# Kernel optimization log

Measured on AMD Instinct MI355X. Metric: run time of the kernel, lower is better.

Reference implementation:

```python
import jax, jax.numpy as jnp
import numpy as np
import math

NUM_LABELS = 8
D_MODEL = 1024
NUM_HEADS = 16
D_PADDED = math.ceil(D_MODEL / NUM_HEADS) * NUM_HEADS  # 1024
D_HEAD = D_PADDED // NUM_HEADS  # 64
B, N = 4, 2048


def setup_inputs() -> dict:
    key = jax.random.key(0)
    ks = jax.random.split(key, 7)
    X = jax.random.normal(ks[0], (B, N, D_MODEL), dtype=jnp.float32)
    L = jax.random.randint(ks[1], (B, N), 0, NUM_LABELS, dtype=jnp.int32)
    # per-label QKV linear params (stored as x @ W + b layout)
    s_in = 1.0 / math.sqrt(D_MODEL)
    Wqkv = jax.random.uniform(ks[2], (NUM_LABELS, D_MODEL, 3 * D_PADDED), jnp.float32, -s_in, s_in)
    bqkv = jax.random.uniform(ks[3], (NUM_LABELS, 3 * D_PADDED), jnp.float32, -s_in, s_in)
    s_p = 1.0 / math.sqrt(D_PADDED)
    Wproj = jax.random.uniform(ks[4], (D_PADDED, D_MODEL), jnp.float32, -s_p, s_p)
    bproj = jax.random.uniform(ks[5], (D_MODEL,), jnp.float32, -s_p, s_p)
    return {"X": X, "L": L, "Wqkv": Wqkv, "bqkv": bqkv, "Wproj": Wproj, "bproj": bproj}


def reference(X, L, Wqkv, bqkv, Wproj, bproj):
    Bb, Nn, _ = X.shape
    # Per-label dense QKV projection, routed by label mask (matches original
    # per-label loop; X_masked zeroing is a no-op on selected positions).
    qkv = jnp.zeros((Bb, Nn, 3 * D_PADDED), dtype=X.dtype)
    for l in range(NUM_LABELS):
        m = (L == l)[..., None]  # [B, N, 1]
        qkv_l = jnp.einsum('bnd,do->bno', X, Wqkv[l]) + bqkv[l]
        qkv = jnp.where(m, qkv_l, qkv)
    q, k, v = jnp.split(qkv, 3, axis=-1)
    # [B, H, N, Dh]
    q = q.reshape(Bb, Nn, NUM_HEADS, D_HEAD).transpose(0, 2, 1, 3)
    k = k.reshape(Bb, Nn, NUM_HEADS, D_HEAD).transpose(0, 2, 1, 3)
    v = v.reshape(Bb, Nn, NUM_HEADS, D_HEAD).transpose(0, 2, 1, 3)
    scores = jnp.einsum('bhnd,bhmd->bhnm', q, k) / math.sqrt(D_HEAD)
    probs = jax.nn.softmax(scores, axis=-1)
    out = jnp.einsum('bhnm,bhmd->bhnd', probs, v)
    out = out.transpose(0, 2, 1, 3).reshape(Bb, Nn, D_PADDED)
    return jnp.einsum('bnd,do->bno', out, Wproj) + bproj
```

## Files before the change

kernel.cpp:

```cpp
#include <hip/hip_runtime.h>
#include <math.h>

#define BATCH 4
#define SEQ   2048
#define TOK   (BATCH * SEQ)
#define DM    1024
#define DP    1024
#define NH    16
#define DH    64
#define NLAB  8
#define QKV_C 3072
#define PADL  1152
#define PROWS (NLAB * PADL)
#define GP    72

typedef __attribute__((ext_vector_type(8))) short bf16x8;
typedef __attribute__((ext_vector_type(4))) float f32x4;

typedef const __attribute__((address_space(1))) void* gas_ptr;
typedef __attribute__((address_space(3))) void* las_ptr;

__device__ __forceinline__ short f2bf(float f) {
  union { float f; unsigned u; } v; v.f = f;
  unsigned r = v.u + 0x7FFF + ((v.u >> 16) & 1);
  return (short)(r >> 16);
}

__device__ __forceinline__ unsigned cvt_pk_bf16(float lo, float hi) {
  unsigned r;
  asm("v_cvt_pk_bf16_f32 %0, %1, %2" : "=v"(r) : "v"(lo), "v"(hi));
  return r;
}

__device__ __forceinline__ float fast_exp2(float x) {
#if __has_builtin(__builtin_amdgcn_exp2f)
  return __builtin_amdgcn_exp2f(x);
#else
  return exp2f(x);
#endif
}

__global__ void build_lists_k(const int* __restrict__ L, int* __restrict__ sorted,
                              int* __restrict__ rowmap) {
  __shared__ int cnt[NLAB], off[NLAB], cur[NLAB];
  int tid = threadIdx.x;
  if (tid < NLAB) cnt[tid] = 0;
  __syncthreads();
  for (int i = tid; i < TOK; i += 256) atomicAdd(&cnt[L[i]], 1);
  __syncthreads();
  if (tid == 0) {
    int o = 0;
    for (int l = 0; l < NLAB; ++l) { off[l] = o; cur[l] = o; o += cnt[l]; }
  }
  __syncthreads();
  for (int i = tid; i < TOK; i += 256) {
    int l = L[i];
    sorted[atomicAdd(&cur[l], 1)] = i;
  }
  __threadfence();
  __syncthreads();
  for (int p = tid; p < PROWS; p += 256) {
    int l = p / PADL, i = p - l * PADL;
    rowmap[p] = (i < cnt[l]) ? sorted[off[l] + i] : -1;
  }
}

__global__ __launch_bounds__(256) void xg_k(const float* __restrict__ X,
                                            const int* __restrict__ rowmap,
                                            short* __restrict__ Xg) {
  int p = blockIdx.x;
  int t = rowmap[p];
  int c = threadIdx.x << 2;
  short* dst = Xg + (size_t)p * DM + c;
  if (t >= 0) {
    float4 v = *(const float4*)(X + (size_t)t * DM + c);
    short tmp[4] = { f2bf(v.x), f2bf(v.y), f2bf(v.z), f2bf(v.w) };
    *(uint2*)dst = *(uint2*)tmp;
  } else {
    uint2 z; z.x = 0u; z.y = 0u;
    *(uint2*)dst = z;
  }
}

__global__ __launch_bounds__(256) void wt_k(const float* __restrict__ src,
                                            short* __restrict__ dst,
                                            int K, int N) {
  __shared__ float Ts[64][65];
  int m = blockIdx.z;
  src += (size_t)m * K * N;
  dst += (size_t)m * (size_t)N * K;
  int n0 = blockIdx.x * 64, k0 = blockIdx.y * 64;
  int tid = threadIdx.x;
  int r = tid >> 4;
  int c = (tid & 15) << 2;
  #pragma unroll
  for (int it = 0; it < 4; ++it) {
    float4 v = *(const float4*)(src + (size_t)(k0 + r + it * 16) * N + n0 + c);
    Ts[c + 0][r + it * 16] = v.x;
    Ts[c + 1][r + it * 16] = v.y;
    Ts[c + 2][r + it * 16] = v.z;
    Ts[c + 3][r + it * 16] = v.w;
  }
  __syncthreads();
  int n = tid >> 2, ks = (tid & 3) << 4;
  short tmp[16];
  #pragma unroll
  for (int j = 0; j < 16; ++j) tmp[j] = f2bf(Ts[n][ks + j]);
  *(bf16x8*)(dst + (size_t)(n0 + n) * K + k0 + ks)     = *(bf16x8*)&tmp[0];
  *(bf16x8*)(dst + (size_t)(n0 + n) * K + k0 + ks + 8) = *(bf16x8*)&tmp[8];
}

__global__ __launch_bounds__(256) void qkv_mfma_k(
    const short* __restrict__ Xg, const short* __restrict__ Wt,
    const float* __restrict__ bqkv, const int* __restrict__ rowmap,
    short* __restrict__ qkvb) {
  __shared__ short As[128 * 64];
  __shared__ short Bs[128 * 64];
  int bx = blockIdx.x, by = blockIdx.y;
  int lab = by / 9;
  int pr0 = by * 128;
  int n0  = bx * 128;
  const short* W = Wt + (size_t)lab * QKV_C * DM;

  int tid  = threadIdx.x;
  int lane = tid & 63, w = tid >> 6;
  int wm = w >> 1, wn = w & 1;
  int col = lane & 15, quad = lane >> 4;

  int lrow = lane >> 3;
  int lcol = (lane & 7) << 3;

  const short* aSrc = Xg + (size_t)(pr0 + w * 32 + lrow) * DM + lcol;
  const short* bSrc = W  + (size_t)(n0  + w * 32 + lrow) * DM + lcol;

  f32x4 acc[4][4];
  #pragma unroll
  for (int mi = 0; mi < 4; ++mi)
    #pragma unroll
    for (int ni = 0; ni < 4; ++ni) acc[mi][ni] = (f32x4){0.f, 0.f, 0.f, 0.f};

  for (int k0 = 0; k0 < DM; k0 += 64) {
    __syncthreads();
    #pragma unroll
    for (int it = 0; it < 4; ++it) {
      __builtin_amdgcn_global_load_lds(
          (gas_ptr)(aSrc + (size_t)(it * 8) * DM + k0),
          (las_ptr)&As[(w * 32 + it * 8) * 64], 16, 0, 0);
      __builtin_amdgcn_global_load_lds(
          (gas_ptr)(bSrc + (size_t)(it * 8) * DM + k0),
          (las_ptr)&Bs[(w * 32 + it * 8) * 64], 16, 0, 0);
    }
    __syncthreads();
    #pragma unroll
    for (int ks = 0; ks < 2; ++ks) {
      bf16x8 a[4], b[4];
      #pragma unroll
      for (int mi = 0; mi < 4; ++mi)
        a[mi] = *(bf16x8*)&As[(wm * 64 + mi * 16 + col) * 64 + ks * 32 + (quad << 3)];
      #pragma unroll
      for (int ni = 0; ni < 4; ++ni)
        b[ni] = *(bf16x8*)&Bs[(wn * 64 + ni * 16 + col) * 64 + ks * 32 + (quad << 3)];
      #pragma unroll
      for (int mi = 0; mi < 4; ++mi)
        #pragma unroll
        for (int ni = 0; ni < 4; ++ni)
          acc[mi][ni] = __builtin_amdgcn_mfma_f32_16x16x32_bf16(a[mi], b[ni], acc[mi][ni], 0, 0, 0);
    }
  }

  float scale = (bx < 8) ? (0.125f * 1.44269504f) : 1.0f;
  const float* bias = bqkv + lab * QKV_C;
  #pragma unroll
  for (int mi = 0; mi < 4; ++mi) {
    #pragma unroll
    for (int r = 0; r < 4; ++r) {
      int prow = pr0 + wm * 64 + mi * 16 + (quad << 2) + r;
      int t2 = rowmap[prow];
      if (t2 < 0) continue;
      #pragma unroll
      for (int ni = 0; ni < 4; ++ni) {
        int gn = n0 + wn * 64 + ni * 16 + col;
        float v = (acc[mi][ni][r] + bias[gn]) * scale;
        qkvb[(size_t)t2 * QKV_C + gn] = f2bf(v);
      }
    }
  }
}

__global__ __launch_bounds__(256) void vtb_k(const short* __restrict__ qkvb,
                                             short* __restrict__ VTg) {
  __shared__ short T[64 * GP];
  int n0 = blockIdx.x * 64, h = blockIdx.y, b = blockIdx.z;
  int tid = threadIdx.x;
  int r = tid >> 2, cb = tid & 3;
  {
    const short* src = qkvb + ((size_t)(b * SEQ + n0 + r)) * QKV_C + 2 * DP + h * DH + (cb << 4);
    int scc = ((cb + (r >> 4)) & 3) << 4;
    *(bf16x8*)&T[r * GP + scc]     = *(const bf16x8*)(src);
    *(bf16x8*)&T[r * GP + scc + 8] = *(const bf16x8*)(src + 8);
  }
  __syncthreads();
  int d = tid >> 2, nc = (tid & 3) << 4;
  int sc2 = (((d >> 4) + (nc >> 4)) & 3) << 4;
  short tmp[16];
  #pragma unroll
  for (int j = 0; j < 16; ++j) tmp[j] = T[(nc + j) * GP + sc2 + (d & 15)];
  short* dst = VTg + ((size_t)(b * NH + h) * DH + d) * SEQ + n0 + nc;
  *(bf16x8*)&dst[0] = *(bf16x8*)&tmp[0];
  *(bf16x8*)&dst[8] = *(bf16x8*)&tmp[8];
}

__global__ __launch_bounds__(256) void attn_k(short* __restrict__ qkvb,
                                              const short* __restrict__ VTg) {
  int qt = blockIdx.x, h = blockIdx.y, b = blockIdx.z;
  __shared__ short Ks[64 * GP];
  __shared__ short VT[64 * GP];
  __shared__ short Ps[128 * GP];

  int tid  = threadIdx.x;
  int lane = tid & 63;
  int w    = tid >> 6;
  int col  = lane & 15;
  int quad = lane >> 4;

  size_t rowbase = (size_t)b * SEQ;
  int hoff = h * DH;
  int sr = tid >> 2;
  int sc = (tid & 3) << 4;

  const short* ksrc = qkvb + (rowbase + sr) * QKV_C + DP + hoff + sc;
  const short* vsrc = VTg + ((size_t)(b * NH + h) * DH + sr) * SEQ + sc;

  bf16x8 qf0[2], qf1[2];
  {
    const short* q0 = qkvb + (rowbase + qt * 128 + (w << 4) + col) * QKV_C + hoff + (quad << 3);
    const short* q1 = q0 + (size_t)64 * QKV_C;
    qf0[0] = *(const bf16x8*)(q0);
    qf0[1] = *(const bf16x8*)(q0 + 32);
    qf1[0] = *(const bf16x8*)(q1);
    qf1[1] = *(const bf16x8*)(q1 + 32);
  }

  {
    bf16x8 ka = *(const bf16x8*)(ksrc);
    bf16x8 kb = *(const bf16x8*)(ksrc + 8);
    bf16x8 va = *(const bf16x8*)(vsrc);
    bf16x8 vb = *(const bf16x8*)(vsrc + 8);
    *(bf16x8*)&Ks[sr * GP + sc]     = ka;
    *(bf16x8*)&Ks[sr * GP + sc + 8] = kb;
    *(bf16x8*)&VT[sr * GP + sc]     = va;
    *(bf16x8*)&VT[sr * GP + sc + 8] = vb;
  }
  __syncthreads();

  float m_0 = -1e30f, l_0 = 0.f, m_1 = -1e30f, l_1 = 0.f;
  f32x4 o0[4], o1[4];
  #pragma unroll
  for (int nd = 0; nd < 4; ++nd) {
    o0[nd] = (f32x4){0.f, 0.f, 0.f, 0.f};
    o1[nd] = (f32x4){0.f, 0.f, 0.f, 0.f};
  }

  short* ps0 = &Ps[((w << 4) + col) * GP];
  short* ps1 = &Ps[(64 + (w << 4) + col) * GP];

  auto softmax_strip = [&](f32x4* s, float& m_, float& l_, f32x4* o, short* psrow) {
    f32x4 t0, t1;
    #pragma unroll
    for (int i = 0; i < 4; ++i) { t0[i] = fmaxf(s[0][i], s[1][i]); t1[i] = fmaxf(s[2][i], s[3][i]); }
    #pragma unroll
    for (int i = 0; i < 4; ++i) t0[i] = fmaxf(t0[i], t1[i]);
    float mx = fmaxf(fmaxf(t0[0], t0[1]), fmaxf(t0[2], t0[3]));
    if (!__all(mx - m_ <= 8.f)) {
      float mxr = fmaxf(mx, __shfl_xor(mx, 16));
      mxr = fmaxf(mxr, __shfl_xor(mxr, 32));
      float mnew  = fmaxf(m_, mxr);
      float alpha = fast_exp2(m_ - mnew);
      l_ *= alpha;
      #pragma unroll
      for (int nd = 0; nd < 4; ++nd)
        #pragma unroll
        for (int r = 0; r < 4; ++r) o[nd][r] *= alpha;
      m_ = mnew;
    }
    float p[4][4];
    #pragma unroll
    for (int nj = 0; nj < 4; ++nj)
      #pragma unroll
      for (int r = 0; r < 4; ++r) p[nj][r] = fast_exp2(s[nj][r] - m_);
    float rs = 0.f;
    #pragma unroll
    for (int nj = 0; nj < 4; ++nj)
      rs += (p[nj][0] + p[nj][1]) + (p[nj][2] + p[nj][3]);
    l_ += rs;
    #pragma unroll
    for (int nj = 0; nj < 4; ++nj) {
      uint2 u;
      u.x = cvt_pk_bf16(p[nj][0], p[nj][1]);
      u.y = cvt_pk_bf16(p[nj][2], p[nj][3]);
      *(uint2*)&psrow[nj * 16 + (quad << 2)] = u;
    }
  };

  auto compute_tile = [&]() {
    f32x4 s0[4], s1[4];
    #pragma unroll
    for (int nj = 0; nj < 4; ++nj) {
      s0[nj] = (f32x4){0.f, 0.f, 0.f, 0.f};
      s1[nj] = (f32x4){0.f, 0.f, 0.f, 0.f};
    }
    __builtin_amdgcn_s_setprio(1);
    #pragma unroll
    for (int ks = 0; ks < 2; ++ks) {
      #pragma unroll
      for (int nj = 0; nj < 4; ++nj) {
        bf16x8 aK = *(bf16x8*)&Ks[((nj << 4) + col) * GP + (ks << 5) + (quad << 3)];
        s0[nj] = __builtin_amdgcn_mfma_f32_16x16x32_bf16(aK, qf0[ks], s0[nj], 0, 0, 0);
        s1[nj] = __builtin_amdgcn_mfma_f32_16x16x32_bf16(aK, qf1[ks], s1[nj], 0, 0, 0);
      }
    }
    __builtin_amdgcn_s_setprio(0);
    softmax_strip(s0, m_0, l_0, o0, ps0);
    softmax_strip(s1, m_1, l_1, o1, ps1);
    __builtin_amdgcn_s_setprio(1);
    #pragma unroll
    for (int ks = 0; ks < 2; ++ks) {
      bf16x8 bP0 = *(bf16x8*)&ps0[(ks << 5) + (quad << 3)];
      bf16x8 bP1 = *(bf16x8*)&ps1[(ks << 5) + (quad << 3)];
      #pragma unroll
      for (int nd = 0; nd < 4; ++nd) {
        bf16x8 aV = *(bf16x8*)&VT[((nd << 4) + col) * GP + (ks << 5) + (quad << 3)];
        o0[nd] = __builtin_amdgcn_mfma_f32_16x16x32_bf16(aV, bP0, o0[nd], 0, 0, 0);
        o1[nd] = __builtin_amdgcn_mfma_f32_16x16x32_bf16(aV, bP1, o1[nd], 0, 0, 0);
      }
    }
    __builtin_amdgcn_s_setprio(0);
  };

  for (int kt = 0; kt < SEQ / 64 - 1; ++kt) {
    const short* kn = ksrc + (size_t)(kt + 1) * 64 * QKV_C;
    const short* vn = vsrc + (size_t)(kt + 1) * 64;
    bf16x8 ka = *(const bf16x8*)(kn);
    bf16x8 kb = *(const bf16x8*)(kn + 8);
    bf16x8 va = *(const bf16x8*)(vn);
    bf16x8 vb = *(const bf16x8*)(vn + 8);

    compute_tile();
    __syncthreads();
    *(bf16x8*)&Ks[sr * GP + sc]     = ka;
    *(bf16x8*)&Ks[sr * GP + sc + 8] = kb;
    *(bf16x8*)&VT[sr * GP + sc]     = va;
    *(bf16x8*)&VT[sr * GP + sc + 8] = vb;
    __syncthreads();
  }
  compute_tile();

  float lt0 = l_0 + __shfl_xor(l_0, 16);
  lt0 += __shfl_xor(lt0, 32);
  float lt1 = l_1 + __shfl_xor(l_1, 16);
  lt1 += __shfl_xor(lt1, 32);
  #pragma unroll
  for (int s = 0; s < 2; ++s) {
    float inv = 1.f / (s ? lt1 : lt0);
    f32x4* o = s ? o1 : o0;
    size_t row = rowbase + qt * 128 + s * 64 + (w << 4) + col;
    #pragma unroll
    for (int nd = 0; nd < 4; ++nd) {
      uint2 u;
      u.x = cvt_pk_bf16(o[nd][0] * inv, o[nd][1] * inv);
      u.y = cvt_pk_bf16(o[nd][2] * inv, o[nd][3] * inv);
      *(uint2*)(qkvb + row * QKV_C + hoff + (nd << 4) + (quad << 2)) = u;
    }
  }
}

__global__ __launch_bounds__(256) void proj_mfma_k(
    const short* __restrict__ Ab, const short* __restrict__ Wt,
    const float* __restrict__ bias, float* __restrict__ out) {
  __shared__ short As[128 * 64];
  __shared__ short Bs[128 * 64];
  int n0 = blockIdx.x * 128, m0 = blockIdx.y * 128;

  int tid  = threadIdx.x;
  int lane = tid & 63, w = tid >> 6;
  int wm = w >> 1, wn = w & 1;
  int col = lane & 15, quad = lane >> 4;

  int lrow = lane >> 3;
  int lcol = (lane & 7) << 3;

  const short* aSrc = Ab + (size_t)(m0 + w * 32 + lrow) * QKV_C + lcol;
  const short* bSrc = Wt + (size_t)(n0 + w * 32 + lrow) * DP + lcol;

  f32x4 acc[4][4];
  #pragma unroll
  for (int mi = 0; mi < 4; ++mi)
    #pragma unroll
    for (int ni = 0; ni < 4; ++ni) acc[mi][ni] = (f32x4){0.f, 0.f, 0.f, 0.f};

  for (int k0 = 0; k0 < DP; k0 += 64) {
    __syncthreads();
    #pragma unroll
    for (int it = 0; it < 4; ++it) {
      __builtin_amdgcn_global_load_lds(
          (gas_ptr)(aSrc + (size_t)(it * 8) * QKV_C + k0),
          (las_ptr)&As[(w * 32 + it * 8) * 64], 16, 0, 0);
      __builtin_amdgcn_global_load_lds(
          (gas_ptr)(bSrc + (size_t)(it * 8) * DP + k0),
          (las_ptr)&Bs[(w * 32 + it * 8) * 64], 16, 0, 0);
    }
    __syncthreads();
    #pragma unroll
    for (int ks = 0; ks < 2; ++ks) {
      bf16x8 a[4], b[4];
      #pragma unroll
      for (int mi = 0; mi < 4; ++mi)
        a[mi] = *(bf16x8*)&As[(wm * 64 + mi * 16 + col) * 64 + ks * 32 + (quad << 3)];
      #pragma unroll
      for (int ni = 0; ni < 4; ++ni)
        b[ni] = *(bf16x8*)&Bs[(wn * 64 + ni * 16 + col) * 64 + ks * 32 + (quad << 3)];
      #pragma unroll
      for (int mi = 0; mi < 4; ++mi)
        #pragma unroll
        for (int ni = 0; ni < 4; ++ni)
          acc[mi][ni] = __builtin_amdgcn_mfma_f32_16x16x32_bf16(a[mi], b[ni], acc[mi][ni], 0, 0, 0);
    }
  }

  #pragma unroll
  for (int mi = 0; mi < 4; ++mi) {
    #pragma unroll
    for (int r = 0; r < 4; ++r) {
      int m = m0 + wm * 64 + mi * 16 + (quad << 2) + r;
      #pragma unroll
      for (int ni = 0; ni < 4; ++ni) {
        int gn = n0 + wn * 64 + ni * 16 + col;
        out[(size_t)m * DM + gn] = acc[mi][ni][r] + bias[gn];
      }
    }
  }
}

extern "C" void kernel_launch(void* const* d_in, const int* in_sizes, int n_in,
                              void* d_out, int out_size, void* d_ws, size_t ws_size,
                              hipStream_t stream) {
  (void)in_sizes; (void)n_in; (void)out_size; (void)ws_size;
  const float* X     = (const float*)d_in[0];
  const int*   L     = (const int*)d_in[1];
  const float* Wqkv  = (const float*)d_in[2];
  const float* bqkv  = (const float*)d_in[3];
  const float* Wproj = (const float*)d_in[4];
  const float* bproj = (const float*)d_in[5];
  float* out = (float*)d_out;

  char* ws = (char*)d_ws;
  short* qkvb    = (short*)ws;
  short* Wqkv_t  = (short*)(ws + (size_t)TOK * QKV_C * 2);
  short* Wproj_t = (short*)(ws + (size_t)TOK * QKV_C * 2
                               + (size_t)NLAB * QKV_C * DM * 2);
  int* sorted = (int*)((char*)Wproj_t + (size_t)DP * DM * 2);
  int* rowmap = sorted + TOK;
  short* Xg = (short*)(rowmap + PROWS);
  short* VTg = Wqkv_t;

  build_lists_k<<<dim3(1), dim3(256), 0, stream>>>(L, sorted, rowmap);
  xg_k<<<dim3(PROWS), dim3(256), 0, stream>>>(X, rowmap, Xg);
  wt_k<<<dim3(QKV_C / 64, DM / 64, NLAB), dim3(256), 0, stream>>>(Wqkv, Wqkv_t, DM, QKV_C);
  wt_k<<<dim3(DM / 64, DP / 64, 1), dim3(256), 0, stream>>>(Wproj, Wproj_t, DP, DM);
  qkv_mfma_k<<<dim3(QKV_C / 128, PROWS / 128), dim3(256), 0, stream>>>(
      Xg, Wqkv_t, bqkv, rowmap, qkvb);
  vtb_k<<<dim3(SEQ / 64, NH, BATCH), dim3(256), 0, stream>>>(qkvb, VTg);
  attn_k<<<dim3(SEQ / 128, NH, BATCH), dim3(256), 0, stream>>>(qkvb, VTg);
  proj_mfma_k<<<dim3(DM / 128, TOK / 128), dim3(256), 0, stream>>>(
      qkvb, Wproj_t, bproj, out);
}
```

Before: 481.6 us.

## Double-buffer LDS tiles and swizzle block order in QKV and projection GEMMs

Both MFMA GEMM kernels now keep two LDS buffers per operand. They prefetch the next K-tile with global_load_lds while computing on the current one, and sync only once per iteration. This hides global-load latency behind MFMA work. The block index is also remapped so that consecutive blocks are spread across the grid, which is meant to improve L2 reuse or XCD distribution. LDS use doubles to 64KB per block, which may reduce occupancy.

```diff
diff --git a/kernel.cpp b/kernel.cpp
--- a/kernel.cpp
+++ b/kernel.cpp
@@ -114,9 +114,11 @@
     const short* __restrict__ Xg, const short* __restrict__ Wt,
     const float* __restrict__ bqkv, const int* __restrict__ rowmap,
     short* __restrict__ qkvb) {
-  __shared__ short As[128 * 64];
-  __shared__ short Bs[128 * 64];
-  int bx = blockIdx.x, by = blockIdx.y;
+  __shared__ short As[2][128 * 64];
+  __shared__ short Bs[2][128 * 64];
+  int flat = blockIdx.y * 24 + blockIdx.x;
+  int swz  = (flat & 7) * 216 + (flat >> 3);
+  int bx = swz % 24, by = swz / 24;
   int lab = by / 9;
   int pr0 = by * 128;
   int n0  = bx * 128;
@@ -139,33 +141,48 @@
     #pragma unroll
     for (int ni = 0; ni < 4; ++ni) acc[mi][ni] = (f32x4){0.f, 0.f, 0.f, 0.f};
 
+  #pragma unroll
+  for (int it = 0; it < 4; ++it) {
+    __builtin_amdgcn_global_load_lds(
+        (gas_ptr)(aSrc + (size_t)(it * 8) * DM),
+        (las_ptr)&As[0][(w * 32 + it * 8) * 64], 16, 0, 0);
+    __builtin_amdgcn_global_load_lds(
+        (gas_ptr)(bSrc + (size_t)(it * 8) * DM),
+        (las_ptr)&Bs[0][(w * 32 + it * 8) * 64], 16, 0, 0);
+  }
+  __syncthreads();
+
+  int cur = 0;
   for (int k0 = 0; k0 < DM; k0 += 64) {
-    __syncthreads();
-    #pragma unroll
-    for (int it = 0; it < 4; ++it) {
-      __builtin_amdgcn_global_load_lds(
-          (gas_ptr)(aSrc + (size_t)(it * 8) * DM + k0),
-          (las_ptr)&As[(w * 32 + it * 8) * 64], 16, 0, 0);
-      __builtin_amdgcn_global_load_lds(
-          (gas_ptr)(bSrc + (size_t)(it * 8) * DM + k0),
-          (las_ptr)&Bs[(w * 32 + it * 8) * 64], 16, 0, 0);
-    }
-    __syncthreads();
+    if (k0 + 64 < DM) {
+      int nxt = cur ^ 1, kn = k0 + 64;
+      #pragma unroll
+      for (int it = 0; it < 4; ++it) {
+        __builtin_amdgcn_global_load_lds(
+            (gas_ptr)(aSrc + (size_t)(it * 8) * DM + kn),
+            (las_ptr)&As[nxt][(w * 32 + it * 8) * 64], 16, 0, 0);
+        __builtin_amdgcn_global_load_lds(
+            (gas_ptr)(bSrc + (size_t)(it * 8) * DM + kn),
+            (las_ptr)&Bs[nxt][(w * 32 + it * 8) * 64], 16, 0, 0);
+      }
+    }
     #pragma unroll
     for (int ks = 0; ks < 2; ++ks) {
       bf16x8 a[4], b[4];
       #pragma unroll
       for (int mi = 0; mi < 4; ++mi)
-        a[mi] = *(bf16x8*)&As[(wm * 64 + mi * 16 + col) * 64 + ks * 32 + (quad << 3)];
+        a[mi] = *(bf16x8*)&As[cur][(wm * 64 + mi * 16 + col) * 64 + ks * 32 + (quad << 3)];
       #pragma unroll
       for (int ni = 0; ni < 4; ++ni)
-        b[ni] = *(bf16x8*)&Bs[(wn * 64 + ni * 16 + col) * 64 + ks * 32 + (quad << 3)];
+        b[ni] = *(bf16x8*)&Bs[cur][(wn * 64 + ni * 16 + col) * 64 + ks * 32 + (quad << 3)];
       #pragma unroll
       for (int mi = 0; mi < 4; ++mi)
         #pragma unroll
         for (int ni = 0; ni < 4; ++ni)
           acc[mi][ni] = __builtin_amdgcn_mfma_f32_16x16x32_bf16(a[mi], b[ni], acc[mi][ni], 0, 0, 0);
     }
+    __syncthreads();
+    cur ^= 1;
   }
 
   float scale = (bx < 8) ? (0.125f * 1.44269504f) : 1.0f;
@@ -377,9 +394,11 @@
 __global__ __launch_bounds__(256) void proj_mfma_k(
     const short* __restrict__ Ab, const short* __restrict__ Wt,
     const float* __restrict__ bias, float* __restrict__ out) {
-  __shared__ short As[128 * 64];
-  __shared__ short Bs[128 * 64];
-  int n0 = blockIdx.x * 128, m0 = blockIdx.y * 128;
+  __shared__ short As[2][128 * 64];
+  __shared__ short Bs[2][128 * 64];
+  int flat = blockIdx.y * 8 + blockIdx.x;
+  int swz  = (flat & 7) * 64 + (flat >> 3);
+  int n0 = (swz & 7) * 128, m0 = (swz >> 3) * 128;
 
   int tid  = threadIdx.x;
   int lane = tid & 63, w = tid >> 6;
@@ -398,33 +417,48 @@
     #pragma unroll
     for (int ni = 0; ni < 4; ++ni) acc[mi][ni] = (f32x4){0.f, 0.f, 0.f, 0.f};
 
+  #pragma unroll
+  for (int it = 0; it < 4; ++it) {
+    __builtin_amdgcn_global_load_lds(
+        (gas_ptr)(aSrc + (size_t)(it * 8) * QKV_C),
+        (las_ptr)&As[0][(w * 32 + it * 8) * 64], 16, 0, 0);
+    __builtin_amdgcn_global_load_lds(
+        (gas_ptr)(bSrc + (size_t)(it * 8) * DP),
+        (las_ptr)&Bs[0][(w * 32 + it * 8) * 64], 16, 0, 0);
+  }
+  __syncthreads();
+
+  int cur = 0;
   for (int k0 = 0; k0 < DP; k0 += 64) {
-    __syncthreads();
-    #pragma unroll
-    for (int it = 0; it < 4; ++it) {
-      __builtin_amdgcn_global_load_lds(
-          (gas_ptr)(aSrc + (size_t)(it * 8) * QKV_C + k0),
-          (las_ptr)&As[(w * 32 + it * 8) * 64], 16, 0, 0);
-      __builtin_amdgcn_global_load_lds(
-          (gas_ptr)(bSrc + (size_t)(it * 8) * DP + k0),
-          (las_ptr)&Bs[(w * 32 + it * 8) * 64], 16, 0, 0);
-    }
-    __syncthreads();
+    if (k0 + 64 < DP) {
+      int nxt = cur ^ 1, kn = k0 + 64;
+      #pragma unroll
+      for (int it = 0; it < 4; ++it) {
+        __builtin_amdgcn_global_load_lds(
+            (gas_ptr)(aSrc + (size_t)(it * 8) * QKV_C + kn),
+            (las_ptr)&As[nxt][(w * 32 + it * 8) * 64], 16, 0, 0);
+        __builtin_amdgcn_global_load_lds(
+            (gas_ptr)(bSrc + (size_t)(it * 8) * DP + kn),
+            (las_ptr)&Bs[nxt][(w * 32 + it * 8) * 64], 16, 0, 0);
+      }
+    }
     #pragma unroll
     for (int ks = 0; ks < 2; ++ks) {
       bf16x8 a[4], b[4];
       #pragma unroll
       for (int mi = 0; mi < 4; ++mi)
-        a[mi] = *(bf16x8*)&As[(wm * 64 + mi * 16 + col) * 64 + ks * 32 + (quad << 3)];
+        a[mi] = *(bf16x8*)&As[cur][(wm * 64 + mi * 16 + col) * 64 + ks * 32 + (quad << 3)];
       #pragma unroll
       for (int ni = 0; ni < 4; ++ni)
-        b[ni] = *(bf16x8*)&Bs[(wn * 64 + ni * 16 + col) * 64 + ks * 32 + (quad << 3)];
+        b[ni] = *(bf16x8*)&Bs[cur][(wn * 64 + ni * 16 + col) * 64 + ks * 32 + (quad << 3)];
       #pragma unroll
       for (int mi = 0; mi < 4; ++mi)
         #pragma unroll
         for (int ni = 0; ni < 4; ++ni)
           acc[mi][ni] = __builtin_amdgcn_mfma_f32_16x16x32_bf16(a[mi], b[ni], acc[mi][ni], 0, 0, 0);
     }
+    __syncthreads();
+    cur ^= 1;
   }
 
   #pragma unroll
```

After: 492.9 us. 2.3% more time.
